# Kernel tuning notes

Hardware: AMD Instinct MI355X
Metric: run time of the kernel (lower is better)

## Reference

```python
import jax, jax.numpy as jnp
import numpy as np

H = 16      # q heads
G = 4       # groups (n_rep)
THETA = 10000.0


def _rope(x, cos, sin):
    # x pairs adjacent elements (torch complex view of reshape(..., -1, 2))
    x0 = x[..., ::2]
    x1 = x[..., 1::2]
    r0 = x0 * cos - x1 * sin
    r1 = x0 * sin + x1 * cos
    return jnp.stack([r0, r1], axis=-1).reshape(x.shape)


def setup_inputs() -> dict:
    key = jax.random.key(0)
    ks = jax.random.split(key, 5)
    B, S, D = 2, 2048, 1024
    return {
        "x": jax.random.normal(ks[0], (B, S, D), jnp.float32),
        "Wq": jax.random.normal(ks[1], (D, D), jnp.float32) * 0.02,
        "Wk": jax.random.normal(ks[2], (D, D // G), jnp.float32) * 0.02,
        "Wv": jax.random.normal(ks[3], (D, D // G), jnp.float32) * 0.02,
        "Wo": jax.random.normal(ks[4], (D, D), jnp.float32) * 0.02,
    }


def reference(x, Wq, Wk, Wv, Wo):
    B, S, D = x.shape
    hd = D // H                     # head dim = 64
    Hkv = H // G                    # kv heads = 4

    q = x @ Wq                      # (B,S,D)
    k = x @ Wk                      # (B,S,D/G)
    v = x @ Wv                      # (B,S,D/G)

    # repeat_kv: (B,S,Hkv,hd) -> (B,S,H,hd)
    k = jnp.repeat(k.reshape(B, S, Hkv, hd), G, axis=2)
    v = jnp.repeat(v.reshape(B, S, Hkv, hd), G, axis=2)

    # RoPE angles: freqs precomputed over hidden_dim (as in source)
    inv = 1.0 / (THETA ** (jnp.arange(0, D, 2, dtype=jnp.float32) / D))  # (D/2,)
    ang = jnp.arange(S, dtype=jnp.float32)[:, None] * inv[None, :]       # (S,D/2)
    q = _rope(q, jnp.cos(ang)[None], jnp.sin(ang)[None])                 # (B,S,D)
    angk = ang[:, : hd // 2]                                             # (S,hd/2)
    k = _rope(k, jnp.cos(angk)[None, :, None, :], jnp.sin(angk)[None, :, None, :])

    q = q.reshape(B, S, H, hd).transpose(0, 2, 1, 3)   # (B,H,S,hd)
    k = k.transpose(0, 2, 1, 3)
    v = v.transpose(0, 2, 1, 3)

    # NOTE: scale uses sqrt(hidden_dim), faithful to source
    scores = jnp.einsum('bhqd,bhkd->bhqk', q, k) / jnp.sqrt(jnp.float32(D))
    p = jax.nn.softmax(scores, axis=-1)
    o = jnp.einsum('bhqk,bhkd->bhqd', p, v)
    o = o.transpose(0, 2, 1, 3).reshape(B, S, D)
    return o @ Wo
```

## Files before the change

### kernel.cpp

```cpp
#include <hip/hip_runtime.h>
#include <math.h>

#define BATCH 2
#define SEQ   2048
#define DMODEL 1024
#define KDIM  1024
#define NH    16
#define HDIM  64
#define GRP   4
#define NKV   4
#define NSPLIT 2

enum { M_PLAIN = 0, M_QKV = 1 };

#define LN_THETA 9.210340371976184f

typedef short bf8_t __attribute__((ext_vector_type(8)));
typedef float f4_t __attribute__((ext_vector_type(4)));
typedef unsigned short us4_t __attribute__((ext_vector_type(4)));
typedef unsigned short us8_t __attribute__((ext_vector_type(8)));

#define QB_OFF 0
#define KB_OFF 4194304
#define VB_OFF (4194304 + 1048576)

__device__ __forceinline__ unsigned short f2bf(float f) {
  unsigned int u = __float_as_uint(f);
  u += 0x7fffu + ((u >> 16) & 1u);
  return (unsigned short)(u >> 16);
}

__device__ __forceinline__ void gload_lds16(const void* g, void* l) {
  typedef __attribute__((address_space(1))) unsigned int gu32;
  typedef __attribute__((address_space(3))) unsigned int lu32;
  __builtin_amdgcn_global_load_lds((const gu32*)g, (lu32*)l, 16, 0, 0);
}

__global__ __launch_bounds__(256) void conv_x(const float* __restrict__ in,
                                              unsigned short* __restrict__ out) {
  const int i = blockIdx.x * 256 + threadIdx.x;
  float4 v = ((const float4*)in)[i];
  us4_t o = {f2bf(v.x), f2bf(v.y), f2bf(v.z), f2bf(v.w)};
  ((us4_t*)out)[i] = o;
}

__global__ __launch_bounds__(256) void convT(const float* __restrict__ W,
                                             unsigned short* __restrict__ out,
                                             int N, int rowoff) {
  __shared__ unsigned short T[64][72];
  const int t = threadIdx.x;
  const int k0 = blockIdx.y * 64, n0 = blockIdx.x * 64;
  const int kr = t >> 4, n4 = (t & 15) * 4;
#pragma unroll
  for (int i = 0; i < 4; ++i) {
    const int k = kr + i * 16;
    float4 v = *(const float4*)&W[(size_t)(k0 + k) * N + n0 + n4];
    T[n4 + 0][k] = f2bf(v.x);
    T[n4 + 1][k] = f2bf(v.y);
    T[n4 + 2][k] = f2bf(v.z);
    T[n4 + 3][k] = f2bf(v.w);
  }
  __syncthreads();
#pragma unroll
  for (int i = 0; i < 2; ++i) {
    const int c = t + i * 256;
    const int n = c >> 3, kc = (c & 7) * 8;
    us8_t v = *(const us8_t*)&T[n][kc];
    *(us8_t*)&out[(size_t)(rowoff + n0 + n) * KDIM + k0 + kc] = v;
  }
}

template <int MODE>
__global__ __launch_bounds__(256, 3) void gemm_bf16(const unsigned short* __restrict__ A,
                                                    const unsigned short* __restrict__ Bt,
                                                    void* __restrict__ Cdst_, int N) {
  __shared__ __align__(16) unsigned short As[64 * 64];
  __shared__ __align__(16) unsigned short Bs[128 * 64];

  const int tid = threadIdx.x;
  const int lane = tid & 63, quad = lane >> 4, l16 = lane & 15;
  const int w = tid >> 6, wm = w >> 1, wn = w & 1;
  const int row0 = blockIdx.x * 64, col0 = blockIdx.y * 128;

  const int m0 = tid >> 2;
  const int kc0 = (tid & 3) ^ ((m0 >> 1) & 3);
  const unsigned short* Ag0 = A + (size_t)(row0 + m0) * KDIM + kc0 * 8;
  const unsigned short* Bg0 = Bt + (size_t)(col0 + m0) * KDIM + kc0 * 8;
  unsigned short* Al0 = &As[tid * 8];
  unsigned short* Bl0 = &Bs[tid * 8];

  int aoff[2][2], boff[4][2];
#pragma unroll
  for (int mi = 0; mi < 2; ++mi) {
    const int am = wm * 32 + mi * 16 + l16;
    const int sw = quad ^ ((am >> 1) & 3);
#pragma unroll
    for (int kh = 0; kh < 2; ++kh)
      aoff[mi][kh] = kh * 2048 + (((am << 2) | sw) << 3);
  }
#pragma unroll
  for (int ni = 0; ni < 4; ++ni) {
    const int bn = wn * 64 + ni * 16 + l16;
    const int sw = quad ^ ((bn >> 1) & 3);
#pragma unroll
    for (int kh = 0; kh < 2; ++kh)
      boff[ni][kh] = kh * 4096 + (((bn << 2) | sw) << 3);
  }

  f4_t acc[2][4];
#pragma unroll
  for (int mi = 0; mi < 2; ++mi)
#pragma unroll
    for (int ni = 0; ni < 4; ++ni) acc[mi][ni] = (f4_t){0.f, 0.f, 0.f, 0.f};

  for (int kb = 0; kb < KDIM; kb += 64) {
    __syncthreads();
    gload_lds16(Ag0 + kb,       Al0);
    gload_lds16(Ag0 + kb + 32,  Al0 + 2048);
    gload_lds16(Bg0 + kb,                     Bl0);
    gload_lds16(Bg0 + (size_t)64 * KDIM + kb, Bl0 + 2048);
    gload_lds16(Bg0 + kb + 32,                     Bl0 + 4096);
    gload_lds16(Bg0 + (size_t)64 * KDIM + kb + 32, Bl0 + 6144);
    __syncthreads();

    bf8_t af[2][2], bfr[4][2];
#pragma unroll
    for (int mi = 0; mi < 2; ++mi)
#pragma unroll
      for (int kh = 0; kh < 2; ++kh) af[mi][kh] = *(const bf8_t*)&As[aoff[mi][kh]];
#pragma unroll
    for (int ni = 0; ni < 4; ++ni)
#pragma unroll
      for (int kh = 0; kh < 2; ++kh) bfr[ni][kh] = *(const bf8_t*)&Bs[boff[ni][kh]];
#pragma unroll
    for (int kh = 0; kh < 2; ++kh)
#pragma unroll
      for (int mi = 0; mi < 2; ++mi)
#pragma unroll
        for (int ni = 0; ni < 4; ++ni)
          acc[mi][ni] = __builtin_amdgcn_mfma_f32_16x16x32_bf16(af[mi][kh], bfr[ni][kh], acc[mi][ni], 0, 0, 0);
  }

  if constexpr (MODE == M_PLAIN) {
    float* out = (float*)Cdst_;
#pragma unroll
    for (int mi = 0; mi < 2; ++mi) {
      const int rowb = row0 + wm * 32 + mi * 16 + quad * 4;
#pragma unroll
      for (int ni = 0; ni < 4; ++ni) {
        const int n = col0 + wn * 64 + ni * 16 + l16;
#pragma unroll
        for (int r = 0; r < 4; ++r)
          out[(size_t)(rowb + r) * N + n] = acc[mi][ni][r];
      }
    }
  } else {
    unsigned short* Qb = (unsigned short*)Cdst_;
    unsigned short* Kb = Qb + (KB_OFF - QB_OFF);
    unsigned short* Vb = Qb + (VB_OFF - QB_OFF);
#pragma unroll
    for (int ni = 0; ni < 4; ++ni) {
      const int nb = col0 + wn * 64 + ni * 16;
      const int n = nb + l16;
      if (nb < 1024) {
        const float inv = expf(-(float)(2 * (n >> 1)) * (LN_THETA / (float)DMODEL));
        const float sgn = (n & 1) ? 1.f : -1.f;
        const int h = n >> 6, d = n & 63;
#pragma unroll
        for (int mi = 0; mi < 2; ++mi) {
          const int rowb = row0 + wm * 32 + mi * 16 + quad * 4;
#pragma unroll
          for (int r = 0; r < 4; ++r) {
            const int row = rowb + r;
            const int bb = row >> 11, s = row & (SEQ - 1);
            const float v = acc[mi][ni][r];
            const float p = __shfl_xor(v, 1);
            float sn, cs;
            sincosf((float)s * inv, &sn, &cs);
            const float res = (v * cs + sgn * p * sn) * 0.03125f;
            Qb[((size_t)(bb * NH + h) * SEQ + s) * HDIM + d] = f2bf(res);
          }
        }
      } else if (nb < 1280) {
        const int nk = n - 1024;
        const int hkv = nk >> 6, d = nk & 63;
        const float inv = expf(-(float)(2 * (d >> 1)) * (LN_THETA / (float)DMODEL));
        const float sgn = (nk & 1) ? 1.f : -1.f;
#pragma unroll
        for (int mi = 0; mi < 2; ++mi) {
          const int rowb = row0 + wm * 32 + mi * 16 + quad * 4;
#pragma unroll
          for (int r = 0; r < 4; ++r) {
            const int row = rowb + r;
            const int bb = row >> 11, s = row & (SEQ - 1);
            const float v = acc[mi][ni][r];
            const float p = __shfl_xor(v, 1);
            float sn, cs;
            sincosf((float)s * inv, &sn, &cs);
            const float res = v * cs + sgn * p * sn;
            Kb[((size_t)(bb * NKV + hkv) * SEQ + s) * HDIM + d] = f2bf(res);
          }
        }
      } else {
        const int nv = n - 1280;
        const int hkv = nv >> 6, d = nv & 63;
#pragma unroll
        for (int mi = 0; mi < 2; ++mi) {
          const int s0 = row0 + wm * 32 + mi * 16 + quad * 4;
          const int bb = s0 >> 11, s = s0 & (SEQ - 1);
          us4_t st = {f2bf(acc[mi][ni][0]), f2bf(acc[mi][ni][1]),
                      f2bf(acc[mi][ni][2]), f2bf(acc[mi][ni][3])};
          *(us4_t*)&Vb[((size_t)(bb * NKV + hkv) * HDIM + d) * SEQ + s] = st;
        }
      }
    }
  }
}

__global__ __launch_bounds__(256, 4) void attn_fwd(const unsigned short* __restrict__ Q,
                                                   const unsigned short* __restrict__ K,
                                                   const unsigned short* __restrict__ V,
                                                   float* __restrict__ Opart,
                                                   float* __restrict__ Lpart) {
  __shared__ __align__(16) unsigned short Kt[4096];
  __shared__ __align__(16) unsigned short Vt[4096];
  __shared__ __align__(16) unsigned short Pt[4][2048];

  const int b = blockIdx.x >> 4;
  const int h = blockIdx.x & (NH - 1);
  const int hkv = h >> 2;
  const int q0 = blockIdx.y * 128;
  const int sp = blockIdx.z;
  const int tid = threadIdx.x;
  const int w = tid >> 6;
  const int lane = tid & 63;
  const int quad = lane >> 4;
  const int l16 = lane & 15;

  const unsigned short* Qg = Q + ((size_t)(b * NH + h) * SEQ + q0 + w * 32) * HDIM;
  const unsigned short* Kg = K + (size_t)(b * NKV + hkv) * SEQ * HDIM;
  const unsigned short* Vg = V + (size_t)(b * NKV + hkv) * HDIM * SEQ;

  bf8_t qb[2][2];
#pragma unroll
  for (int g = 0; g < 2; ++g)
#pragma unroll
    for (int half = 0; half < 2; ++half)
      qb[g][half] = *(const bf8_t*)(Qg + (size_t)(g * 16 + l16) * HDIM + half * 32 + quad * 8);

  bf8_t ones;
#pragma unroll
  for (int i = 0; i < 8; ++i) ones[i] = (short)0x3F80;

  f4_t accO[2][4];
#pragma unroll
  for (int g = 0; g < 2; ++g)
#pragma unroll
    for (int d = 0; d < 4; ++d) accO[g][d] = (f4_t){0.f, 0.f, 0.f, 0.f};
  f4_t accL[2] = {(f4_t){0.f, 0.f, 0.f, 0.f}, (f4_t){0.f, 0.f, 0.f, 0.f}};

  const int x7 = l16 & 7;
  const int kc0 = (quad ^ x7) << 3;
  const int kc1 = kc0 ^ 32;
  unsigned short* Ptw = Pt[w];

  const int srow = tid >> 3;
  const int sch = tid & 7;

  const int kbeg = sp * (SEQ / NSPLIT);
  const int kend = kbeg + SEQ / NSPLIT;
  for (int k0 = kbeg; k0 < kend; k0 += 64) {
    __syncthreads();
#pragma unroll
    for (int i = 0; i < 2; ++i) {
      const int row = srow + i * 32;
      const int pcol = ((sch ^ (row & 7)) << 3);
      *(bf8_t*)&Kt[row * 64 + pcol] = *(const bf8_t*)(Kg + (size_t)(k0 + row) * HDIM + sch * 8);
      *(bf8_t*)&Vt[row * 64 + pcol] = *(const bf8_t*)(Vg + (size_t)row * SEQ + k0 + sch * 8);
    }
    __syncthreads();

#pragma unroll
    for (int cb = 0; cb < 4; ++cb) {
      const int krow = (cb * 16 + l16) * 64;
      bf8_t kf0 = *(const bf8_t*)&Kt[krow + kc0];
      bf8_t kf1 = *(const bf8_t*)&Kt[krow + kc1];
      const int pcol = (((cb * 2 + (quad >> 1)) ^ x7) << 3) + ((quad & 1) << 2);
#pragma unroll
      for (int g = 0; g < 2; ++g) {
        f4_t s = (f4_t){0.f, 0.f, 0.f, 0.f};
        s = __builtin_amdgcn_mfma_f32_16x16x32_bf16(kf0, qb[g][0], s, 0, 0, 0);
        s = __builtin_amdgcn_mfma_f32_16x16x32_bf16(kf1, qb[g][1], s, 0, 0, 0);
        us4_t p = {f2bf(__expf(s[0])), f2bf(__expf(s[1])),
                   f2bf(__expf(s[2])), f2bf(__expf(s[3]))};
        *(us4_t*)&Ptw[(g * 16 + l16) * 64 + pcol] = p;
      }
    }

    bf8_t pa[2][2];
#pragma unroll
    for (int g = 0; g < 2; ++g) {
      const int prow = (g * 16 + l16) * 64;
      pa[g][0] = *(const bf8_t*)&Ptw[prow + kc0];
      pa[g][1] = *(const bf8_t*)&Ptw[prow + kc1];
      accL[g] = __builtin_amdgcn_mfma_f32_16x16x32_bf16(pa[g][0], ones, accL[g], 0, 0, 0);
      accL[g] = __builtin_amdgcn_mfma_f32_16x16x32_bf16(pa[g][1], ones, accL[g], 0, 0, 0);
    }

#pragma unroll
    for (int db = 0; db < 4; ++db) {
      const int vrow = (db * 16 + l16) * 64;
      bf8_t vf0 = *(const bf8_t*)&Vt[vrow + kc0];
      bf8_t vf1 = *(const bf8_t*)&Vt[vrow + kc1];
#pragma unroll
      for (int g = 0; g < 2; ++g) {
        accO[g][db] = __builtin_amdgcn_mfma_f32_16x16x32_bf16(pa[g][0], vf0, accO[g][db], 0, 0, 0);
        accO[g][db] = __builtin_amdgcn_mfma_f32_16x16x32_bf16(pa[g][1], vf1, accO[g][db], 0, 0, 0);
      }
    }
  }

  float* Osp = Opart + (size_t)sp * BATCH * SEQ * NH * HDIM;
  float* Lsp = Lpart + (size_t)sp * BATCH * SEQ * NH;
#pragma unroll
  for (int g = 0; g < 2; ++g)
#pragma unroll
    for (int r = 0; r < 4; ++r) {
      const int q = q0 + w * 32 + g * 16 + quad * 4 + r;
      const size_t rowi = ((size_t)b * SEQ + q) * NH + h;
      float* op = Osp + rowi * HDIM;
#pragma unroll
      for (int db = 0; db < 4; ++db)
        op[db * 16 + l16] = accO[g][db][r];
      if (l16 == 0) Lsp[rowi] = accL[g][r];
    }
}

__global__ __launch_bounds__(256) void attn_merge(const float* __restrict__ Opart,
                                                  const float* __restrict__ Lpart,
                                                  unsigned short* __restrict__ Ow) {
  const int idx = blockIdx.x * 256 + threadIdx.x;
  const int g = idx >> 4, j = (idx & 15) * 4;
  const size_t nq = (size_t)BATCH * SEQ * NH;
  float4 o0 = *(const float4*)&Opart[(size_t)g * HDIM + j];
  float4 o1 = *(const float4*)&Opart[nq * HDIM + (size_t)g * HDIM + j];
  const float il = 1.0f / (Lpart[g] + Lpart[nq + g]);
  us4_t o = {f2bf((o0.x + o1.x) * il), f2bf((o0.y + o1.y) * il),
             f2bf((o0.z + o1.z) * il), f2bf((o0.w + o1.w) * il)};
  *(us4_t*)&Ow[(size_t)g * HDIM + j] = o;
}

extern "C" void kernel_launch(void* const* d_in, const int* in_sizes, int n_in,
                              void* d_out, int out_size, void* d_ws, size_t ws_size,
                              hipStream_t stream) {
  (void)in_sizes; (void)n_in; (void)out_size; (void)ws_size;
  const float* x  = (const float*)d_in[0];
  const float* Wq = (const float*)d_in[1];
  const float* Wk = (const float*)d_in[2];
  const float* Wv = (const float*)d_in[3];
  const float* Wo = (const float*)d_in[4];
  float* out = (float*)d_out;

  unsigned short* Qb    = (unsigned short*)d_ws;
  unsigned short* Kb    = Qb + 4194304;
  unsigned short* Vb    = Kb + 1048576;
  unsigned short* xb    = Vb + 1048576;
  unsigned short* Owb   = xb + 4194304;
  unsigned short* Wqkvt = Owb + 4194304;
  unsigned short* Wot   = Wqkvt + 1572864;
  float* Opart = (float*)(Wot + 1048576);
  float* Lpart = Opart + (size_t)NSPLIT * 4194304;

  dim3 blk(256);
  conv_x<<<dim3(4096), blk, 0, stream>>>(x, xb);
  convT<<<dim3(16, 16), blk, 0, stream>>>(Wq, Wqkvt, DMODEL, 0);
  convT<<<dim3(4, 16), blk, 0, stream>>>(Wk, Wqkvt, DMODEL / GRP, 1024);
  convT<<<dim3(4, 16), blk, 0, stream>>>(Wv, Wqkvt, DMODEL / GRP, 1280);
  convT<<<dim3(16, 16), blk, 0, stream>>>(Wo, Wot, DMODEL, 0);

  gemm_bf16<M_QKV><<<dim3(64, 12), blk, 0, stream>>>(xb, Wqkvt, Qb, 1536);
  attn_fwd<<<dim3(BATCH * NH, SEQ / 128, NSPLIT), blk, 0, stream>>>(Qb, Kb, Vb, Opart, Lpart);
  attn_merge<<<dim3(4096), blk, 0, stream>>>(Opart, Lpart, Owb);
  gemm_bf16<M_PLAIN><<<dim3(64, 8), blk, 0, stream>>>(Owb, Wot, out, DMODEL);
}
```

Before: 185.5 us.

## Merge weight conversions, async-load K/V to LDS, sum softmax denominator in registers

The four weight transpose/convert launches are folded into one kernel indexed by blockIdx.z, with early exit for the narrower K/V weights. In attention, K/V tile staging uses global_load_lds direct-to-LDS copies with swizzled source addresses instead of register round trips. The row-sum MFMAs against a ones vector are replaced by scalar accumulation of the exponentials plus a cross-lane shuffle reduction at the end. bf16 packing of P now uses a perm-based round-half-up instead of round-to-nearest-even, which slightly changes rounding; an unused LDS readback of L is left in.

```diff
diff --git a/kernel.cpp b/kernel.cpp
--- a/kernel.cpp
+++ b/kernel.cpp
@@ -44,12 +44,24 @@
   ((us4_t*)out)[i] = o;
 }
 
-__global__ __launch_bounds__(256) void convT(const float* __restrict__ W,
-                                             unsigned short* __restrict__ out,
-                                             int N, int rowoff) {
+__global__ __launch_bounds__(256) void convT_all(const float* __restrict__ W0,
+                                                 const float* __restrict__ W1,
+                                                 const float* __restrict__ W2,
+                                                 const float* __restrict__ W3,
+                                                 unsigned short* __restrict__ Wqkvt,
+                                                 unsigned short* __restrict__ Wot) {
+  const float* W; unsigned short* out; int N, rowoff;
+  switch (blockIdx.z) {
+    case 0: W = W0; out = Wqkvt; N = 1024; rowoff = 0;    break;
+    case 1: W = W1; out = Wqkvt; N = 256;  rowoff = 1024; break;
+    case 2: W = W2; out = Wqkvt; N = 256;  rowoff = 1280; break;
+    default: W = W3; out = Wot;  N = 1024; rowoff = 0;    break;
+  }
+  const int n0 = blockIdx.x * 64;
+  if (n0 >= N) return;
   __shared__ unsigned short T[64][72];
   const int t = threadIdx.x;
-  const int k0 = blockIdx.y * 64, n0 = blockIdx.x * 64;
+  const int k0 = blockIdx.y * 64;
   const int kr = t >> 4, n4 = (t & 15) * 4;
 #pragma unroll
   for (int i = 0; i < 4; ++i) {
@@ -248,36 +260,31 @@
     for (int half = 0; half < 2; ++half)
       qb[g][half] = *(const bf8_t*)(Qg + (size_t)(g * 16 + l16) * HDIM + half * 32 + quad * 8);
 
-  bf8_t ones;
-#pragma unroll
-  for (int i = 0; i < 8; ++i) ones[i] = (short)0x3F80;
-
   f4_t accO[2][4];
 #pragma unroll
   for (int g = 0; g < 2; ++g)
 #pragma unroll
     for (int d = 0; d < 4; ++d) accO[g][d] = (f4_t){0.f, 0.f, 0.f, 0.f};
-  f4_t accL[2] = {(f4_t){0.f, 0.f, 0.f, 0.f}, (f4_t){0.f, 0.f, 0.f, 0.f}};
+  float accLs[2] = {0.f, 0.f};
 
   const int x7 = l16 & 7;
   const int kc0 = (quad ^ x7) << 3;
   const int kc1 = kc0 ^ 32;
   unsigned short* Ptw = Pt[w];
 
-  const int srow = tid >> 3;
-  const int sch = tid & 7;
+  const int srow0 = tid >> 3, sch = tid & 7;
+  const int gcol = ((sch ^ (srow0 & 7)) << 3);
+  const unsigned short* KgA = Kg + (size_t)srow0 * HDIM + gcol;
+  const unsigned short* VgA = Vg + (size_t)srow0 * SEQ + gcol;
 
   const int kbeg = sp * (SEQ / NSPLIT);
   const int kend = kbeg + SEQ / NSPLIT;
   for (int k0 = kbeg; k0 < kend; k0 += 64) {
     __syncthreads();
-#pragma unroll
-    for (int i = 0; i < 2; ++i) {
-      const int row = srow + i * 32;
-      const int pcol = ((sch ^ (row & 7)) << 3);
-      *(bf8_t*)&Kt[row * 64 + pcol] = *(const bf8_t*)(Kg + (size_t)(k0 + row) * HDIM + sch * 8);
-      *(bf8_t*)&Vt[row * 64 + pcol] = *(const bf8_t*)(Vg + (size_t)row * SEQ + k0 + sch * 8);
-    }
+    gload_lds16(KgA + (size_t)k0 * HDIM, &Kt[tid * 8]);
+    gload_lds16(KgA + (size_t)(k0 + 32) * HDIM, &Kt[tid * 8 + 2048]);
+    gload_lds16(VgA + k0, &Vt[tid * 8]);
+    gload_lds16(VgA + k0 + 32 * SEQ, &Vt[tid * 8 + 2048]);
     __syncthreads();
 
 #pragma unroll
@@ -291,9 +298,15 @@
         f4_t s = (f4_t){0.f, 0.f, 0.f, 0.f};
         s = __builtin_amdgcn_mfma_f32_16x16x32_bf16(kf0, qb[g][0], s, 0, 0, 0);
         s = __builtin_amdgcn_mfma_f32_16x16x32_bf16(kf1, qb[g][1], s, 0, 0, 0);
-        us4_t p = {f2bf(__expf(s[0])), f2bf(__expf(s[1])),
-                   f2bf(__expf(s[2])), f2bf(__expf(s[3]))};
-        *(us4_t*)&Ptw[(g * 16 + l16) * 64 + pcol] = p;
+        const float p0 = __expf(s[0]), p1 = __expf(s[1]);
+        const float p2 = __expf(s[2]), p3 = __expf(s[3]);
+        accLs[g] += (p0 + p1) + (p2 + p3);
+        uint2 pk;
+        pk.x = __builtin_amdgcn_perm(__float_as_uint(p1) + 0x8000u,
+                                     __float_as_uint(p0) + 0x8000u, 0x07060302u);
+        pk.y = __builtin_amdgcn_perm(__float_as_uint(p3) + 0x8000u,
+                                     __float_as_uint(p2) + 0x8000u, 0x07060302u);
+        *(uint2*)&Ptw[(g * 16 + l16) * 64 + pcol] = pk;
       }
     }
 
@@ -303,10 +316,7 @@
       const int prow = (g * 16 + l16) * 64;
       pa[g][0] = *(const bf8_t*)&Ptw[prow + kc0];
       pa[g][1] = *(const bf8_t*)&Ptw[prow + kc1];
-      accL[g] = __builtin_amdgcn_mfma_f32_16x16x32_bf16(pa[g][0], ones, accL[g], 0, 0, 0);
-      accL[g] = __builtin_amdgcn_mfma_f32_16x16x32_bf16(pa[g][1], ones, accL[g], 0, 0, 0);
-    }
-
+    }
 #pragma unroll
     for (int db = 0; db < 4; ++db) {
       const int vrow = (db * 16 + l16) * 64;
@@ -320,6 +330,20 @@
     }
   }
 
+#pragma unroll
+  for (int g = 0; g < 2; ++g) {
+    accLs[g] += __shfl_xor(accLs[g], 16);
+    accLs[g] += __shfl_xor(accLs[g], 32);
+  }
+  float* Lsh = (float*)Ptw;
+  if (quad == 0) {
+    Lsh[l16] = accLs[0];
+    Lsh[16 + l16] = accLs[1];
+  }
+  float4 lrow[2];
+  lrow[0] = *(const float4*)&Lsh[quad * 4];
+  lrow[1] = *(const float4*)&Lsh[16 + quad * 4];
+
   float* Osp = Opart + (size_t)sp * BATCH * SEQ * NH * HDIM;
   float* Lsp = Lpart + (size_t)sp * BATCH * SEQ * NH;
 #pragma unroll
@@ -332,8 +356,15 @@
 #pragma unroll
       for (int db = 0; db < 4; ++db)
         op[db * 16 + l16] = accO[g][db][r];
-      if (l16 == 0) Lsp[rowi] = accL[g][r];
-    }
+      (void)lrow;
+    }
+  if (quad == 0) {
+#pragma unroll
+    for (int g = 0; g < 2; ++g) {
+      const int q = q0 + w * 32 + g * 16 + l16;
+      Lsp[((size_t)b * SEQ + q) * NH + h] = accLs[g];
+    }
+  }
 }
 
 __global__ __launch_bounds__(256) void attn_merge(const float* __restrict__ Opart,
@@ -373,10 +404,7 @@
 
   dim3 blk(256);
   conv_x<<<dim3(4096), blk, 0, stream>>>(x, xb);
-  convT<<<dim3(16, 16), blk, 0, stream>>>(Wq, Wqkvt, DMODEL, 0);
-  convT<<<dim3(4, 16), blk, 0, stream>>>(Wk, Wqkvt, DMODEL / GRP, 1024);
-  convT<<<dim3(4, 16), blk, 0, stream>>>(Wv, Wqkvt, DMODEL / GRP, 1280);
-  convT<<<dim3(16, 16), blk, 0, stream>>>(Wo, Wot, DMODEL, 0);
+  convT_all<<<dim3(16, 16, 4), blk, 0, stream>>>(Wq, Wk, Wv, Wo, Wqkvt, Wot);
 
   gemm_bf16<M_QKV><<<dim3(64, 12), blk, 0, stream>>>(xb, Wqkvt, Qb, 1536);
   attn_fwd<<<dim3(BATCH * NH, SEQ / 128, NSPLIT), blk, 0, stream>>>(Qb, Kb, Vb, Opart, Lpart);
```

Result: faster. 178.1 us (-4.0%).
